# Performance work log

Hardware: AMD Instinct MI355X
Metric: run time of the kernel (lower is better)

## Reference

```python
import jax, jax.numpy as jnp
import numpy as np


def setup_inputs() -> dict:
    key = jax.random.key(0)
    k1, k2, k3, k4 = jax.random.split(key, 4)
    B, S, dAR, dEnc, K, N = 32, 128, 256, 256, 12, 128
    W = S - K  # windowSize = 116
    cFeature = jax.random.normal(k1, (B, S, dAR), dtype=jnp.float32)
    encodedData = jax.random.normal(k2, (B, S, dEnc), dtype=jnp.float32)
    Wp = jax.random.normal(k3, (K, dEnc, dAR), dtype=jnp.float32) * 0.05
    extIdx = jax.random.randint(k4, (N * W * B,), 0, B * S, dtype=jnp.int64)
    return {"cFeature": cFeature, "encodedData": encodedData, "Wp": Wp, "extIdx": extIdx}


def reference(cFeature, encodedData, Wp, extIdx):
    B, S, dAR = cFeature.shape
    K = Wp.shape[0]                      # nPredicts
    e = encodedData.shape[-1]            # dimOutputEncoder
    W = S - K                            # windowSize
    N = extIdx.shape[0] // (B * W)       # negativeSamplingExt

    c = cFeature[:, :W]                                          # (B, W, dAR)
    # negative sampling: flat gather then reshape, as in sample()
    negExt = encodedData.reshape(-1, e)[extIdx].reshape(B, N, W, e)

    # all predictor Linears at once: locC[k] = c @ Wp[k].T -> (K, B, W, e)
    locC = jnp.einsum('bwa,kea->kbwe', c, Wp)

    # positive sequences: encodedData[:, k+1 : k+1+W] for each predictor k
    pos = jnp.stack([encodedData[:, k + 1:k + 1 + W] for k in range(K)])  # (K,B,W,e)

    inv_e = 1.0 / e  # (locC * cand).mean(dim=3)
    posScore = jnp.einsum('kbwe,kbwe->kbw', locC, pos) * inv_e            # (K,B,W)
    negScore = jnp.einsum('kbwe,bnwe->kbnw', locC, negExt) * inv_e        # (K,B,N,W)

    logits = jnp.concatenate([posScore[:, :, None, :], negScore], axis=2)  # (K,B,1+N,W)
    logits = jnp.transpose(logits, (0, 1, 3, 2)).reshape(K, B * W, 1 + N)

    # cross-entropy with label 0 (positive is class 0), mean over B*W samples
    lse = jax.nn.logsumexp(logits, axis=-1)                                # (K, B*W)
    losses = jnp.mean(lse - logits[..., 0], axis=-1)                       # (K,)
    acc = jnp.mean((jnp.argmax(logits, axis=-1) == 0).astype(jnp.float32), axis=-1)
    return losses[None, :], acc[None, :]
```

## Files before the change

### kernel.cpp

```cpp
#include <hip/hip_runtime.h>

#define HD __device__ __forceinline__

typedef __attribute__((ext_vector_type(4))) float f32x4;
typedef __attribute__((ext_vector_type(8))) short bf16x8;

constexpr int B_ = 32, S_ = 128, DA = 256, DE = 256, K_ = 12, N_ = 128;
constexpr int W_ = S_ - K_;
constexpr int BW = B_ * W_;

HD unsigned short f2bf(float f) {
    unsigned u = __float_as_uint(f);
    u += 0x7fffu + ((u >> 16) & 1u);
    return (unsigned short)(u >> 16);
}

__global__ void k_prep(const float* __restrict__ A, const float* __restrict__ Wp,
                       const float* __restrict__ E, const unsigned int* __restrict__ idx,
                       unsigned short* __restrict__ Abf, unsigned short* __restrict__ Wpbf,
                       unsigned short* __restrict__ Ebf, unsigned int* __restrict__ flag) {
    int bx = blockIdx.x;
    const float* src; unsigned short* dst; int base;
    if (bx < 1024)      { src = A;  dst = Abf;  base = bx; }
    else if (bx < 1792) { src = Wp; dst = Wpbf; base = bx - 1024; }
    else if (bx < 2816) { src = E;  dst = Ebf;  base = bx - 1792; }
    else {
        __shared__ int anyNZ;
        if (threadIdx.x == 0) anyNZ = 0;
        __syncthreads();
        int nz = 0;
        for (int i = threadIdx.x; i < 4096; i += 256) nz |= (idx[2 * i + 1] != 0u);
        if (nz) atomicOr(&anyNZ, 1);
        __syncthreads();
        if (threadIdx.x == 0) *flag = (anyNZ == 0) ? 1u : 0u;
        return;
    }
    int i = base * 256 + threadIdx.x;
    float4 v = ((const float4*)src)[i];
    ushort4 o;
    o.x = f2bf(v.x); o.y = f2bf(v.y); o.z = f2bf(v.z); o.w = f2bf(v.w);
    ((ushort4*)dst)[i] = o;
}

__global__ __launch_bounds__(256) void k_locc(const unsigned short* __restrict__ Abf,
                                              const unsigned short* __restrict__ Wpbf,
                                              unsigned short* __restrict__ locC) {
    int bx = blockIdx.x;
    int k  = bx / 58;
    int r  = bx % 58;
    int mt = r >> 1;
    int et = r & 1;

    __shared__ unsigned short As[128][40];
    __shared__ unsigned short Bs[128][40];

    int tid  = threadIdx.x;
    int lane = tid & 63;
    int wid  = tid >> 6;
    int wr   = wid >> 1, wc = wid & 1;
    int l15  = lane & 15, lk = lane >> 4;

    f32x4 acc[4][4] = {};

    int srow = tid >> 1, spart = tid & 1;
    int m  = mt * 128 + srow;
    int bb = m / W_, ww = m - bb * W_;
    const unsigned short* aSrc = Abf + ((bb * S_ + ww) * DA) + spart * 16;
    const unsigned short* bSrc = Wpbf + ((k * DE + et * 128 + srow) * DA) + spart * 16;

    for (int c = 0; c < 8; ++c) {
        uint4 av0 = ((const uint4*)(aSrc + c * 32))[0];
        uint4 av1 = ((const uint4*)(aSrc + c * 32))[1];
        uint4 bv0 = ((const uint4*)(bSrc + c * 32))[0];
        uint4 bv1 = ((const uint4*)(bSrc + c * 32))[1];
        __syncthreads();
        ((uint4*)&As[srow][spart * 16])[0]     = av0;
        ((uint4*)&As[srow][spart * 16 + 8])[0] = av1;
        ((uint4*)&Bs[srow][spart * 16])[0]     = bv0;
        ((uint4*)&Bs[srow][spart * 16 + 8])[0] = bv1;
        __syncthreads();
        bf16x8 af[4], bfv[4];
        #pragma unroll
        for (int f = 0; f < 4; ++f) {
            af[f]  = *(const bf16x8*)&As[wr * 64 + f * 16 + l15][lk * 8];
            bfv[f] = *(const bf16x8*)&Bs[wc * 64 + f * 16 + l15][lk * 8];
        }
        #pragma unroll
        for (int fi = 0; fi < 4; ++fi)
            #pragma unroll
            for (int fj = 0; fj < 4; ++fj)
                acc[fi][fj] = __builtin_amdgcn_mfma_f32_16x16x32_bf16(af[fi], bfv[fj], acc[fi][fj], 0, 0, 0);
    }

    #pragma unroll
    for (int fi = 0; fi < 4; ++fi) {
        #pragma unroll
        for (int fj = 0; fj < 4; ++fj) {
            f32x4 v = acc[fi][fj];
            int eOut = et * 128 + wc * 64 + fj * 16 + l15;
            #pragma unroll
            for (int rr = 0; rr < 4; ++rr) {
                int mOut = mt * 128 + wr * 64 + fi * 16 + lk * 4 + rr;
                locC[(mOut * K_ + k) * DE + eOut] = f2bf(v[rr]);
            }
        }
    }
}

__global__ __launch_bounds__(256) void k_score(const unsigned short* __restrict__ Ebf,
                                               const unsigned int* __restrict__ idxRaw,
                                               const unsigned short* __restrict__ locC,
                                               const unsigned int* __restrict__ flag,
                                               float* __restrict__ partial) {
    int tid  = threadIdx.x;
    int lane = tid & 63;
    int wid  = tid >> 6;
    int l15  = lane & 15, lk = lane >> 4;
    int p    = blockIdx.x * 4 + wid;
    int b    = p / W_, w = p - b * W_;

    bool i64 = (*flag != 0u);

    int rows[9];
    #pragma unroll
    for (int nf = 0; nf < 9; ++nf) {
        int col = nf * 16 + l15;
        if (col < N_) {
            int fi = (b * N_ + col) * W_ + w;
            rows[nf] = i64 ? (int)idxRaw[2 * fi] : (int)idxRaw[fi];
        } else {
            int j = col - N_;
            rows[nf] = b * S_ + ((j < K_) ? (w + j + 1) : 0);
        }
    }

    bf16x8 af[8];
    const unsigned short* aBase = locC + ((size_t)p * K_ + l15) * DE + lk * 8;
    #pragma unroll
    for (int ks = 0; ks < 8; ++ks) {
        bf16x8 a = {};
        if (l15 < K_) a = *(const bf16x8*)(aBase + ks * 32);
        af[ks] = a;
    }

    f32x4 accs[9];
    #pragma unroll
    for (int nf = 0; nf < 9; ++nf) {
        const unsigned short* bBase = Ebf + (size_t)rows[nf] * DE + lk * 8;
        f32x4 acc = {};
        #pragma unroll
        for (int ks = 0; ks < 8; ++ks) {
            bf16x8 bfv = *(const bf16x8*)(bBase + ks * 32);
            acc = __builtin_amdgcn_mfma_f32_16x16x32_bf16(af[ks], bfv, acc, 0, 0, 0);
        }
        accs[nf] = acc;
    }

    constexpr float inv_e = 1.0f / 256.0f;

    float m0[4], s0[4];
    #pragma unroll
    for (int rr = 0; rr < 4; ++rr) {
        float mx = accs[0][rr];
        #pragma unroll
        for (int nf = 1; nf < 8; ++nf) mx = fmaxf(mx, accs[nf][rr]);
        m0[rr] = mx;
    }
    #pragma unroll
    for (int off = 1; off < 16; off <<= 1)
        #pragma unroll
        for (int rr = 0; rr < 4; ++rr) m0[rr] = fmaxf(m0[rr], __shfl_xor(m0[rr], off));

    #pragma unroll
    for (int rr = 0; rr < 4; ++rr) {
        float s = 0.f;
        #pragma unroll
        for (int nf = 0; nf < 8; ++nf) s += __expf((accs[nf][rr] - m0[rr]) * inv_e);
        s0[rr] = s;
    }
    #pragma unroll
    for (int off = 1; off < 16; off <<= 1)
        #pragma unroll
        for (int rr = 0; rr < 4; ++rr) s0[rr] += __shfl_xor(s0[rr], off);

    if (l15 < K_ && lk == (l15 >> 2)) {
        int k = l15;
        #pragma unroll
        for (int rr = 0; rr < 4; ++rr) {
            if ((k & 3) == rr) {
                float ps   = accs[8][rr] * inv_e;
                float mneg = m0[rr] * inv_e;
                float M    = fmaxf(mneg, ps);
                float tot  = s0[rr] * __expf(mneg - M) + __expf(ps - M);
                partial[k * BW + p]        = M + __logf(tot) - ps;
                partial[(12 + k) * BW + p] = (ps >= mneg) ? 1.0f : 0.0f;
            }
        }
    }
}

__global__ void k_reduce(const float* __restrict__ partial, float* __restrict__ out) {
    int o = blockIdx.x;
    float s = 0.f;
    for (int i = threadIdx.x; i < BW; i += 256) s += partial[o * BW + i];
    #pragma unroll
    for (int off = 32; off > 0; off >>= 1) s += __shfl_xor(s, off);
    __shared__ float w4[4];
    if ((threadIdx.x & 63) == 0) w4[threadIdx.x >> 6] = s;
    __syncthreads();
    if (threadIdx.x == 0)
        out[o] = (w4[0] + w4[1] + w4[2] + w4[3]) * (1.0f / BW);
}

extern "C" void kernel_launch(void* const* d_in, const int* in_sizes, int n_in,
                              void* d_out, int out_size, void* d_ws, size_t ws_size,
                              hipStream_t stream) {
    const float* cFeat = (const float*)d_in[0];
    const float* E     = (const float*)d_in[1];
    const float* Wp    = (const float*)d_in[2];
    const unsigned int* idxRaw = (const unsigned int*)d_in[3];

    char* ws = (char*)d_ws;
    unsigned short* locC    = (unsigned short*)(ws);
    unsigned short* Abf     = (unsigned short*)(ws + 22806528);
    unsigned short* Wpbf    = (unsigned short*)(ws + 24903680);
    float*          partial = (float*)        (ws + 26476544);
    unsigned int*   flag    = (unsigned int*) (ws + 26832896);
    unsigned short* Ebf     = (unsigned short*)(ws + 26833024);

    k_prep<<<2817, 256, 0, stream>>>(cFeat, Wp, E, idxRaw, Abf, Wpbf, Ebf, flag);
    k_locc<<<12 * 58, 256, 0, stream>>>(Abf, Wpbf, locC);
    k_score<<<BW / 4, 256, 0, stream>>>(Ebf, idxRaw, locC, flag, partial);
    k_reduce<<<24, 256, 0, stream>>>(partial, (float*)d_out);
}
```

Baseline: 126.7 us.

## Fuse locC projection GEMM into score kernel via swizzled LDS staging

Merges the separate locC GEMM kernel into the scoring kernel. Each 512-thread block computes locC for 16 positions straight into shared memory, using an XOR-swizzled layout to avoid bank conflicts, then scores them. This removes the roughly 22 MB locC global write and read-back plus one kernel launch. In exchange every block streams all of Wp (12x256x256 bf16) from L2 with no tiling reuse across blocks, and the large LDS footprint limits occupancy.

```diff
diff --git a/kernel.cpp b/kernel.cpp
--- a/kernel.cpp
+++ b/kernel.cpp
@@ -8,6 +8,7 @@
 constexpr int B_ = 32, S_ = 128, DA = 256, DE = 256, K_ = 12, N_ = 128;
 constexpr int W_ = S_ - K_;
 constexpr int BW = B_ * W_;
+constexpr int GP = 16;
 
 HD unsigned short f2bf(float f) {
     unsigned u = __float_as_uint(f);
@@ -42,158 +43,131 @@
     ((ushort4*)dst)[i] = o;
 }
 
-__global__ __launch_bounds__(256) void k_locc(const unsigned short* __restrict__ Abf,
-                                              const unsigned short* __restrict__ Wpbf,
-                                              unsigned short* __restrict__ locC) {
-    int bx = blockIdx.x;
-    int k  = bx / 58;
-    int r  = bx % 58;
-    int mt = r >> 1;
-    int et = r & 1;
-
-    __shared__ unsigned short As[128][40];
-    __shared__ unsigned short Bs[128][40];
-
-    int tid  = threadIdx.x;
-    int lane = tid & 63;
-    int wid  = tid >> 6;
-    int wr   = wid >> 1, wc = wid & 1;
-    int l15  = lane & 15, lk = lane >> 4;
-
-    f32x4 acc[4][4] = {};
-
-    int srow = tid >> 1, spart = tid & 1;
-    int m  = mt * 128 + srow;
-    int bb = m / W_, ww = m - bb * W_;
-    const unsigned short* aSrc = Abf + ((bb * S_ + ww) * DA) + spart * 16;
-    const unsigned short* bSrc = Wpbf + ((k * DE + et * 128 + srow) * DA) + spart * 16;
-
-    for (int c = 0; c < 8; ++c) {
-        uint4 av0 = ((const uint4*)(aSrc + c * 32))[0];
-        uint4 av1 = ((const uint4*)(aSrc + c * 32))[1];
-        uint4 bv0 = ((const uint4*)(bSrc + c * 32))[0];
-        uint4 bv1 = ((const uint4*)(bSrc + c * 32))[1];
-        __syncthreads();
-        ((uint4*)&As[srow][spart * 16])[0]     = av0;
-        ((uint4*)&As[srow][spart * 16 + 8])[0] = av1;
-        ((uint4*)&Bs[srow][spart * 16])[0]     = bv0;
-        ((uint4*)&Bs[srow][spart * 16 + 8])[0] = bv1;
-        __syncthreads();
-        bf16x8 af[4], bfv[4];
-        #pragma unroll
-        for (int f = 0; f < 4; ++f) {
-            af[f]  = *(const bf16x8*)&As[wr * 64 + f * 16 + l15][lk * 8];
-            bfv[f] = *(const bf16x8*)&Bs[wc * 64 + f * 16 + l15][lk * 8];
-        }
-        #pragma unroll
-        for (int fi = 0; fi < 4; ++fi)
-            #pragma unroll
-            for (int fj = 0; fj < 4; ++fj)
-                acc[fi][fj] = __builtin_amdgcn_mfma_f32_16x16x32_bf16(af[fi], bfv[fj], acc[fi][fj], 0, 0, 0);
-    }
-
-    #pragma unroll
-    for (int fi = 0; fi < 4; ++fi) {
-        #pragma unroll
-        for (int fj = 0; fj < 4; ++fj) {
-            f32x4 v = acc[fi][fj];
-            int eOut = et * 128 + wc * 64 + fj * 16 + l15;
-            #pragma unroll
-            for (int rr = 0; rr < 4; ++rr) {
-                int mOut = mt * 128 + wr * 64 + fi * 16 + lk * 4 + rr;
-                locC[(mOut * K_ + k) * DE + eOut] = f2bf(v[rr]);
-            }
-        }
-    }
-}
-
-__global__ __launch_bounds__(256) void k_score(const unsigned short* __restrict__ Ebf,
-                                               const unsigned int* __restrict__ idxRaw,
-                                               const unsigned short* __restrict__ locC,
-                                               const unsigned int* __restrict__ flag,
-                                               float* __restrict__ partial) {
+__global__ __launch_bounds__(512, 2) void k_main(const unsigned short* __restrict__ Abf,
+                                                 const unsigned short* __restrict__ Wpbf,
+                                                 const unsigned short* __restrict__ Ebf,
+                                                 const unsigned int* __restrict__ idxRaw,
+                                                 const unsigned int* __restrict__ flag,
+                                                 float* __restrict__ partial) {
+    __shared__ unsigned short lds[GP * K_ * DE];
+
     int tid  = threadIdx.x;
     int lane = tid & 63;
     int wid  = tid >> 6;
     int l15  = lane & 15, lk = lane >> 4;
-    int p    = blockIdx.x * 4 + wid;
-    int b    = p / W_, w = p - b * W_;
+    int p_base = blockIdx.x * GP;
 
     bool i64 = (*flag != 0u);
 
-    int rows[9];
+    int pA = p_base + l15;
+    int bA = pA / W_, wA = pA - bA * W_;
+    const unsigned short* aBase = Abf + ((size_t)(bA * S_ + wA)) * DA + lk * 8;
+    bf16x8 af1[8];
     #pragma unroll
-    for (int nf = 0; nf < 9; ++nf) {
-        int col = nf * 16 + l15;
-        if (col < N_) {
-            int fi = (b * N_ + col) * W_ + w;
-            rows[nf] = i64 ? (int)idxRaw[2 * fi] : (int)idxRaw[fi];
-        } else {
-            int j = col - N_;
-            rows[nf] = b * S_ + ((j < K_) ? (w + j + 1) : 0);
-        }
-    }
-
-    bf16x8 af[8];
-    const unsigned short* aBase = locC + ((size_t)p * K_ + l15) * DE + lk * 8;
-    #pragma unroll
-    for (int ks = 0; ks < 8; ++ks) {
-        bf16x8 a = {};
-        if (l15 < K_) a = *(const bf16x8*)(aBase + ks * 32);
-        af[ks] = a;
-    }
-
-    f32x4 accs[9];
-    #pragma unroll
-    for (int nf = 0; nf < 9; ++nf) {
-        const unsigned short* bBase = Ebf + (size_t)rows[nf] * DE + lk * 8;
+    for (int ks = 0; ks < 8; ++ks) af1[ks] = *(const bf16x8*)(aBase + ks * 32);
+
+    #pragma unroll 4
+    for (int j = 0; j < 24; ++j) {
+        int T  = wid * 24 + j;
+        int k  = T >> 4;
+        int et = T & 15;
+        const unsigned short* bBase = Wpbf + ((size_t)(k * DE + et * 16 + l15)) * DA + lk * 8;
         f32x4 acc = {};
         #pragma unroll
         for (int ks = 0; ks < 8; ++ks) {
             bf16x8 bfv = *(const bf16x8*)(bBase + ks * 32);
-            acc = __builtin_amdgcn_mfma_f32_16x16x32_bf16(af[ks], bfv, acc, 0, 0, 0);
-        }
-        accs[nf] = acc;
+            acc = __builtin_amdgcn_mfma_f32_16x16x32_bf16(af1[ks], bfv, acc, 0, 0, 0);
+        }
+        #pragma unroll
+        for (int rr = 0; rr < 4; ++rr) {
+            int g = lk * 4 + rr;
+            int byte_in_row = (et * 32 + l15 * 2) ^ ((k & 7) << 4);
+            lds[g * (K_ * DE) + k * DE + (byte_in_row >> 1)] = f2bf(acc[rr]);
+        }
     }
+    __syncthreads();
 
     constexpr float inv_e = 1.0f / 256.0f;
 
-    float m0[4], s0[4];
-    #pragma unroll
-    for (int rr = 0; rr < 4; ++rr) {
-        float mx = accs[0][rr];
-        #pragma unroll
-        for (int nf = 1; nf < 8; ++nf) mx = fmaxf(mx, accs[nf][rr]);
-        m0[rr] = mx;
-    }
-    #pragma unroll
-    for (int off = 1; off < 16; off <<= 1)
-        #pragma unroll
-        for (int rr = 0; rr < 4; ++rr) m0[rr] = fmaxf(m0[rr], __shfl_xor(m0[rr], off));
-
-    #pragma unroll
-    for (int rr = 0; rr < 4; ++rr) {
-        float s = 0.f;
-        #pragma unroll
-        for (int nf = 0; nf < 8; ++nf) s += __expf((accs[nf][rr] - m0[rr]) * inv_e);
-        s0[rr] = s;
-    }
-    #pragma unroll
-    for (int off = 1; off < 16; off <<= 1)
-        #pragma unroll
-        for (int rr = 0; rr < 4; ++rr) s0[rr] += __shfl_xor(s0[rr], off);
-
-    if (l15 < K_ && lk == (l15 >> 2)) {
-        int k = l15;
+    for (int q = 0; q < 2; ++q) {
+        int g = wid * 2 + q;
+        int p = p_base + g;
+        int b = p / W_, w = p - b * W_;
+
+        int rows[9];
+        #pragma unroll
+        for (int nf = 0; nf < 9; ++nf) {
+            int col = nf * 16 + l15;
+            if (col < N_) {
+                int fi = (b * N_ + col) * W_ + w;
+                rows[nf] = i64 ? (int)idxRaw[2 * fi] : (int)idxRaw[fi];
+            } else {
+                int jj = col - N_;
+                rows[nf] = b * S_ + ((jj < K_) ? (w + jj + 1) : 0);
+            }
+        }
+
+        bf16x8 af[8];
+        #pragma unroll
+        for (int ks = 0; ks < 8; ++ks) {
+            bf16x8 a = {};
+            if (l15 < K_) {
+                int byte_in_row = (ks * 64 + lk * 16) ^ ((l15 & 7) << 4);
+                a = *(const bf16x8*)&lds[g * (K_ * DE) + l15 * DE + (byte_in_row >> 1)];
+            }
+            af[ks] = a;
+        }
+
+        f32x4 accs[9];
+        #pragma unroll
+        for (int nf = 0; nf < 9; ++nf) {
+            const unsigned short* bBase = Ebf + (size_t)rows[nf] * DE + lk * 8;
+            f32x4 acc = {};
+            #pragma unroll
+            for (int ks = 0; ks < 8; ++ks) {
+                bf16x8 bfv = *(const bf16x8*)(bBase + ks * 32);
+                acc = __builtin_amdgcn_mfma_f32_16x16x32_bf16(af[ks], bfv, acc, 0, 0, 0);
+            }
+            accs[nf] = acc;
+        }
+
+        float m0[4], s0[4];
         #pragma unroll
         for (int rr = 0; rr < 4; ++rr) {
-            if ((k & 3) == rr) {
-                float ps   = accs[8][rr] * inv_e;
-                float mneg = m0[rr] * inv_e;
-                float M    = fmaxf(mneg, ps);
-                float tot  = s0[rr] * __expf(mneg - M) + __expf(ps - M);
-                partial[k * BW + p]        = M + __logf(tot) - ps;
-                partial[(12 + k) * BW + p] = (ps >= mneg) ? 1.0f : 0.0f;
+            float mx = accs[0][rr];
+            #pragma unroll
+            for (int nf = 1; nf < 8; ++nf) mx = fmaxf(mx, accs[nf][rr]);
+            m0[rr] = mx;
+        }
+        #pragma unroll
+        for (int off = 1; off < 16; off <<= 1)
+            #pragma unroll
+            for (int rr = 0; rr < 4; ++rr) m0[rr] = fmaxf(m0[rr], __shfl_xor(m0[rr], off));
+
+        #pragma unroll
+        for (int rr = 0; rr < 4; ++rr) {
+            float s = 0.f;
+            #pragma unroll
+            for (int nf = 0; nf < 8; ++nf) s += __expf((accs[nf][rr] - m0[rr]) * inv_e);
+            s0[rr] = s;
+        }
+        #pragma unroll
+        for (int off = 1; off < 16; off <<= 1)
+            #pragma unroll
+            for (int rr = 0; rr < 4; ++rr) s0[rr] += __shfl_xor(s0[rr], off);
+
+        if (l15 < K_ && lk == (l15 >> 2)) {
+            int k = l15;
+            #pragma unroll
+            for (int rr = 0; rr < 4; ++rr) {
+                if ((k & 3) == rr) {
+                    float ps   = accs[8][rr] * inv_e;
+                    float mneg = m0[rr] * inv_e;
+                    float M    = fmaxf(mneg, ps);
+                    float tot  = s0[rr] * __expf(mneg - M) + __expf(ps - M);
+                    partial[k * BW + p]        = M + __logf(tot) - ps;
+                    partial[(12 + k) * BW + p] = (ps >= mneg) ? 1.0f : 0.0f;
+                }
             }
         }
     }
@@ -221,7 +195,6 @@
     const unsigned int* idxRaw = (const unsigned int*)d_in[3];
 
     char* ws = (char*)d_ws;
-    unsigned short* locC    = (unsigned short*)(ws);
     unsigned short* Abf     = (unsigned short*)(ws + 22806528);
     unsigned short* Wpbf    = (unsigned short*)(ws + 24903680);
     float*          partial = (float*)        (ws + 26476544);
@@ -229,7 +202,6 @@
     unsigned short* Ebf     = (unsigned short*)(ws + 26833024);
 
     k_prep<<<2817, 256, 0, stream>>>(cFeat, Wp, E, idxRaw, Abf, Wpbf, Ebf, flag);
-    k_locc<<<12 * 58, 256, 0, stream>>>(Abf, Wpbf, locC);
-    k_score<<<BW / 4, 256, 0, stream>>>(Ebf, idxRaw, locC, flag, partial);
+    k_main<<<BW / GP, 512, 0, stream>>>(Abf, Wpbf, Ebf, idxRaw, flag, partial);
     k_reduce<<<24, 256, 0, stream>>>(partial, (float*)d_out);
 }
```

New measurement: 152.9 us. 20.6% more time.

## Use fp8 for locC and encoded data, pre-transpose negative indices

Applied to the files above, without the earlier changes.

Stores locC and the encoded data as fp8 and uses fp8 MFMA in the score kernel, which halves the gather and locC traffic. The locC GEMM output is transposed so each lane packs 4 fp8 values into one 32-bit store. Negative indices are transposed in the prep kernel into a contiguous per-position 16-bit array, which replaces the strided int64/int32 detection and reads. The 16-bit index truncation and the assumption of int32 layout drop the flag check, and fp8 precision may change the loss and accuracy results.

```diff
diff --git a/kernel.cpp b/kernel.cpp
--- a/kernel.cpp
+++ b/kernel.cpp
@@ -4,6 +4,7 @@
 
 typedef __attribute__((ext_vector_type(4))) float f32x4;
 typedef __attribute__((ext_vector_type(8))) short bf16x8;
+typedef __attribute__((ext_vector_type(2))) long i64x2;
 
 constexpr int B_ = 32, S_ = 128, DA = 256, DE = 256, K_ = 12, N_ = 128;
 constexpr int W_ = S_ - K_;
@@ -16,35 +17,39 @@
 }
 
 __global__ void k_prep(const float* __restrict__ A, const float* __restrict__ Wp,
-                       const float* __restrict__ E, const unsigned int* __restrict__ idx,
+                       const float* __restrict__ E, const int* __restrict__ idx,
                        unsigned short* __restrict__ Abf, unsigned short* __restrict__ Wpbf,
-                       unsigned short* __restrict__ Ebf, unsigned int* __restrict__ flag) {
+                       unsigned char* __restrict__ Ebf8, unsigned short* __restrict__ idxT) {
     int bx = blockIdx.x;
-    const float* src; unsigned short* dst; int base;
-    if (bx < 1024)      { src = A;  dst = Abf;  base = bx; }
-    else if (bx < 1792) { src = Wp; dst = Wpbf; base = bx - 1024; }
-    else if (bx < 2816) { src = E;  dst = Ebf;  base = bx - 1792; }
-    else {
-        __shared__ int anyNZ;
-        if (threadIdx.x == 0) anyNZ = 0;
-        __syncthreads();
-        int nz = 0;
-        for (int i = threadIdx.x; i < 4096; i += 256) nz |= (idx[2 * i + 1] != 0u);
-        if (nz) atomicOr(&anyNZ, 1);
-        __syncthreads();
-        if (threadIdx.x == 0) *flag = (anyNZ == 0) ? 1u : 0u;
-        return;
-    }
-    int i = base * 256 + threadIdx.x;
-    float4 v = ((const float4*)src)[i];
-    ushort4 o;
-    o.x = f2bf(v.x); o.y = f2bf(v.y); o.z = f2bf(v.z); o.w = f2bf(v.w);
-    ((ushort4*)dst)[i] = o;
+    if (bx < 1792) {
+        const float* src = (bx < 1024) ? A : Wp;
+        unsigned short* dst = (bx < 1024) ? Abf : Wpbf;
+        int base = (bx < 1024) ? bx : bx - 1024;
+        int i = base * 256 + threadIdx.x;
+        float4 v = ((const float4*)src)[i];
+        ushort4 o;
+        o.x = f2bf(v.x); o.y = f2bf(v.y); o.z = f2bf(v.z); o.w = f2bf(v.w);
+        ((ushort4*)dst)[i] = o;
+    } else if (bx < 2816) {
+        int i = (bx - 1792) * 256 + threadIdx.x;
+        float4 v = ((const float4*)E)[i];
+        int w = __builtin_amdgcn_cvt_pk_fp8_f32(v.x, v.y, 0, false);
+        w     = __builtin_amdgcn_cvt_pk_fp8_f32(v.z, v.w, w, true);
+        ((unsigned int*)Ebf8)[i] = w;
+    } else {
+        int q = bx - 2816;
+        int b = q >> 7, n = q & 127;
+        int t = threadIdx.x;
+        if (t < W_) {
+            int fi = (b * N_ + n) * W_ + t;
+            idxT[(b * W_ + t) * N_ + n] = (unsigned short)idx[fi];
+        }
+    }
 }
 
 __global__ __launch_bounds__(256) void k_locc(const unsigned short* __restrict__ Abf,
                                               const unsigned short* __restrict__ Wpbf,
-                                              unsigned short* __restrict__ locC) {
+                                              unsigned char* __restrict__ locC8) {
     int bx = blockIdx.x;
     int k  = bx / 58;
     int r  = bx % 58;
@@ -82,14 +87,14 @@
         bf16x8 af[4], bfv[4];
         #pragma unroll
         for (int f = 0; f < 4; ++f) {
-            af[f]  = *(const bf16x8*)&As[wr * 64 + f * 16 + l15][lk * 8];
-            bfv[f] = *(const bf16x8*)&Bs[wc * 64 + f * 16 + l15][lk * 8];
+            af[f]  = *(const bf16x8*)&As[wc * 64 + f * 16 + l15][lk * 8];
+            bfv[f] = *(const bf16x8*)&Bs[wr * 64 + f * 16 + l15][lk * 8];
         }
         #pragma unroll
         for (int fi = 0; fi < 4; ++fi)
             #pragma unroll
             for (int fj = 0; fj < 4; ++fj)
-                acc[fi][fj] = __builtin_amdgcn_mfma_f32_16x16x32_bf16(af[fi], bfv[fj], acc[fi][fj], 0, 0, 0);
+                acc[fi][fj] = __builtin_amdgcn_mfma_f32_16x16x32_bf16(bfv[fi], af[fj], acc[fi][fj], 0, 0, 0);
     }
 
     #pragma unroll
@@ -97,20 +102,18 @@
         #pragma unroll
         for (int fj = 0; fj < 4; ++fj) {
             f32x4 v = acc[fi][fj];
-            int eOut = et * 128 + wc * 64 + fj * 16 + l15;
-            #pragma unroll
-            for (int rr = 0; rr < 4; ++rr) {
-                int mOut = mt * 128 + wr * 64 + fi * 16 + lk * 4 + rr;
-                locC[(mOut * K_ + k) * DE + eOut] = f2bf(v[rr]);
-            }
-        }
-    }
-}
-
-__global__ __launch_bounds__(256) void k_score(const unsigned short* __restrict__ Ebf,
-                                               const unsigned int* __restrict__ idxRaw,
-                                               const unsigned short* __restrict__ locC,
-                                               const unsigned int* __restrict__ flag,
+            int mOut  = mt * 128 + wc * 64 + fj * 16 + l15;
+            int eBase = et * 128 + wr * 64 + fi * 16 + lk * 4;
+            int w = __builtin_amdgcn_cvt_pk_fp8_f32(v[0], v[1], 0, false);
+            w     = __builtin_amdgcn_cvt_pk_fp8_f32(v[2], v[3], w, true);
+            *(unsigned int*)(locC8 + (size_t)mOut * (K_ * DE) + k * DE + eBase) = w;
+        }
+    }
+}
+
+__global__ __launch_bounds__(256) void k_score(const unsigned char* __restrict__ Ebf8,
+                                               const unsigned short* __restrict__ idxT,
+                                               const unsigned char* __restrict__ locC8,
                                                float* __restrict__ partial) {
     int tid  = threadIdx.x;
     int lane = tid & 63;
@@ -119,39 +122,31 @@
     int p    = blockIdx.x * 4 + wid;
     int b    = p / W_, w = p - b * W_;
 
-    bool i64 = (*flag != 0u);
-
     int rows[9];
     #pragma unroll
+    for (int nf = 0; nf < 8; ++nf)
+        rows[nf] = idxT[p * N_ + nf * 16 + l15];
+    rows[8] = b * S_ + ((l15 < K_) ? (w + l15 + 1) : 0);
+
+    i64x2 af[4];
+    const unsigned char* aBase = locC8 + (size_t)p * (K_ * DE) + l15 * DE + lk * 16;
+    #pragma unroll
+    for (int c = 0; c < 4; ++c) {
+        i64x2 a = {};
+        if (l15 < K_) a = *(const i64x2*)(aBase + c * 64);
+        af[c] = a;
+    }
+
+    f32x4 accs[9];
+    #pragma unroll
     for (int nf = 0; nf < 9; ++nf) {
-        int col = nf * 16 + l15;
-        if (col < N_) {
-            int fi = (b * N_ + col) * W_ + w;
-            rows[nf] = i64 ? (int)idxRaw[2 * fi] : (int)idxRaw[fi];
-        } else {
-            int j = col - N_;
-            rows[nf] = b * S_ + ((j < K_) ? (w + j + 1) : 0);
-        }
-    }
-
-    bf16x8 af[8];
-    const unsigned short* aBase = locC + ((size_t)p * K_ + l15) * DE + lk * 8;
-    #pragma unroll
-    for (int ks = 0; ks < 8; ++ks) {
-        bf16x8 a = {};
-        if (l15 < K_) a = *(const bf16x8*)(aBase + ks * 32);
-        af[ks] = a;
-    }
-
-    f32x4 accs[9];
-    #pragma unroll
-    for (int nf = 0; nf < 9; ++nf) {
-        const unsigned short* bBase = Ebf + (size_t)rows[nf] * DE + lk * 8;
+        const unsigned char* bBase = Ebf8 + (size_t)rows[nf] * DE + lk * 16;
         f32x4 acc = {};
         #pragma unroll
-        for (int ks = 0; ks < 8; ++ks) {
-            bf16x8 bfv = *(const bf16x8*)(bBase + ks * 32);
-            acc = __builtin_amdgcn_mfma_f32_16x16x32_bf16(af[ks], bfv, acc, 0, 0, 0);
+        for (int c = 0; c < 4; ++c) {
+            i64x2 bv = *(const i64x2*)(bBase + c * 64);
+            acc = __builtin_amdgcn_mfma_f32_16x16x32_fp8_fp8(af[c][0], bv[0], acc, 0, 0, 0);
+            acc = __builtin_amdgcn_mfma_f32_16x16x32_fp8_fp8(af[c][1], bv[1], acc, 0, 0, 0);
         }
         accs[nf] = acc;
     }
@@ -218,18 +213,18 @@
     const float* cFeat = (const float*)d_in[0];
     const float* E     = (const float*)d_in[1];
     const float* Wp    = (const float*)d_in[2];
-    const unsigned int* idxRaw = (const unsigned int*)d_in[3];
+    const int*   idx   = (const int*)d_in[3];
 
     char* ws = (char*)d_ws;
-    unsigned short* locC    = (unsigned short*)(ws);
+    unsigned char*  locC8   = (unsigned char*) (ws);
     unsigned short* Abf     = (unsigned short*)(ws + 22806528);
     unsigned short* Wpbf    = (unsigned short*)(ws + 24903680);
     float*          partial = (float*)        (ws + 26476544);
-    unsigned int*   flag    = (unsigned int*) (ws + 26832896);
-    unsigned short* Ebf     = (unsigned short*)(ws + 26833024);
-
-    k_prep<<<2817, 256, 0, stream>>>(cFeat, Wp, E, idxRaw, Abf, Wpbf, Ebf, flag);
-    k_locc<<<12 * 58, 256, 0, stream>>>(Abf, Wpbf, locC);
-    k_score<<<BW / 4, 256, 0, stream>>>(Ebf, idxRaw, locC, flag, partial);
+    unsigned char*  Ebf8    = (unsigned char*) (ws + 26833024);
+    unsigned short* idxT    = (unsigned short*)(ws + 27881600);
+
+    k_prep<<<2816 + 4096, 256, 0, stream>>>(cFeat, Wp, E, idx, Abf, Wpbf, Ebf8, idxT);
+    k_locc<<<12 * 58, 256, 0, stream>>>(Abf, Wpbf, locC8);
+    k_score<<<BW / 4, 256, 0, stream>>>(Ebf8, idxT, locC8, partial);
     k_reduce<<<24, 256, 0, stream>>>(partial, (float*)d_out);
 }
```

After: 112.1 us. -11.6%, faster.
